# Kernel tuning notes

Hardware: AMD Instinct MI355X
Metric: run time of the kernel (lower is better)

The kernel has to match this reference:

```python
import jax, jax.numpy as jnp
import numpy as np

LEVELS = 2
BS = 8                 # block_size == plane_h == plane_w
NORMALS = (0, 1, 2)    # axis-aligned plane normals within each block
TAU = 0.05
INV_SQRT2 = 0.7071067811865476

# ---------- 1D orthonormal Haar along an axis ----------

def _dwt1(x, axis):
    x = jnp.moveaxis(x, axis, -1)
    a, b = x[..., 0::2], x[..., 1::2]
    lo = (a + b) * INV_SQRT2
    hi = (a - b) * INV_SQRT2
    return jnp.moveaxis(lo, -1, axis), jnp.moveaxis(hi, -1, axis)


def _idwt1(lo, hi, axis):
    lo = jnp.moveaxis(lo, axis, -1)
    hi = jnp.moveaxis(hi, axis, -1)
    even = (lo + hi) * INV_SQRT2
    odd = (lo - hi) * INV_SQRT2
    y = jnp.stack([even, odd], axis=-1).reshape(lo.shape[:-1] + (lo.shape[-1] * 2,))
    return jnp.moveaxis(y, -1, axis)

# ---------- one level of separable 3D Haar (8 subbands) ----------

def _dwt3_level(x):
    ld, hd = _dwt1(x, -3)
    out = {}
    for dn, db in (('l', ld), ('h', hd)):
        lh, hh = _dwt1(db, -2)
        for hn, hb in (('l', lh), ('h', hh)):
            lw, hw = _dwt1(hb, -1)
            out[dn + hn + 'l'] = lw
            out[dn + hn + 'h'] = hw
    return out


def _idwt3_level(bands):
    rec_h = {dn + hn: _idwt1(bands[dn + hn + 'l'], bands[dn + hn + 'h'], -1)
             for dn in 'lh' for hn in 'lh'}
    rec_d = {dn: _idwt1(rec_h[dn + 'l'], rec_h[dn + 'h'], -2) for dn in 'lh'}
    return _idwt1(rec_d['l'], rec_d['h'], -3)

# ---------- full multi-level 2D Haar on the last two dims (planes) ----------

def _haar2_fwd(p):
    s = p.shape[-1]
    out = p
    while s > 1:
        sub = out[..., :s, :s]
        a, b = sub[..., 0::2, :], sub[..., 1::2, :]
        sub = jnp.concatenate([(a + b) * INV_SQRT2, (a - b) * INV_SQRT2], axis=-2)
        a, b = sub[..., :, 0::2], sub[..., :, 1::2]
        sub = jnp.concatenate([(a + b) * INV_SQRT2, (a - b) * INV_SQRT2], axis=-1)
        out = out.at[..., :s, :s].set(sub)
        s //= 2
    return out


def _haar2_inv(c):
    s_full = c.shape[-1]
    out = c
    s = 2
    while s <= s_full:
        sub = out[..., :s, :s]
        lo, hi = sub[..., :, :s // 2], sub[..., :, s // 2:]
        even = (lo + hi) * INV_SQRT2
        odd = (lo - hi) * INV_SQRT2
        sub = jnp.stack([even, odd], axis=-1).reshape(sub.shape[:-1] + (s,))
        lo, hi = sub[..., :s // 2, :], sub[..., s // 2:, :]
        even = (lo + hi) * INV_SQRT2
        odd = (lo - hi) * INV_SQRT2
        sub = jnp.stack([even, odd], axis=-2).reshape(sub.shape[:-2] + (s, s))
        out = out.at[..., :s, :s].set(sub)
        s *= 2
    return out

# ---------- block extraction / assembly ----------

def _extract_blocks(band, bs):
    B, C, D, H, W = band.shape
    pd, ph, pw = (-D) % bs, (-H) % bs, (-W) % bs
    band = jnp.pad(band, ((0, 0), (0, 0), (0, pd), (0, ph), (0, pw)), mode='edge')
    nd, nh, nw = (D + pd) // bs, (H + ph) // bs, (W + pw) // bs
    blk = band.reshape(B, C, nd, bs, nh, bs, nw, bs).transpose(0, 1, 2, 4, 6, 3, 5, 7)
    return blk.reshape(-1, bs, bs, bs), (B, C, D, H, W), (nd, nh, nw)


def _assemble_blocks(blocks, orig, nblk, bs):
    B, C, D, H, W = orig
    nd, nh, nw = nblk
    x = blocks.reshape(B, C, nd, nh, nw, bs, bs, bs).transpose(0, 1, 2, 5, 3, 6, 4, 7)
    x = x.reshape(B, C, nd * bs, nh * bs, nw * bs)
    return x[:, :, :D, :H, :W]

# ---------- planewise bandlet analysis / synthesis ----------

def _analyze(blocks):
    # for each normal axis n: slice cube into planes perpendicular to n, 2D Haar each plane
    return jnp.stack([_haar2_fwd(jnp.moveaxis(blocks, 1 + n, 1)) for n in NORMALS], axis=1)


def _synthesize(packed):
    recs = [jnp.moveaxis(_haar2_inv(packed[:, i]), 1, 1 + n) for i, n in enumerate(NORMALS)]
    acc = recs[0]
    for r in recs[1:]:
        acc = acc + r
    return acc / len(NORMALS)


def _soft_threshold(c, tau):
    dc = c[..., 0, 0]  # keep per-plane DC coefficient
    t = jnp.sign(c) * jnp.maximum(jnp.abs(c) - tau, 0.0)
    return t.at[..., 0, 0].set(dc)

# ---------- full encode -> threshold -> reconstruct ----------

def _forward(x):
    B, C, D, H, W = x.shape
    mult = 2 ** LEVELS
    pd, ph, pw = (-D) % mult, (-H) % mult, (-W) % mult
    xp = jnp.pad(x, ((0, 0), (0, 0), (0, pd), (0, ph), (0, pw)), mode='reflect')
    approx = xp
    levels = []
    for _ in range(LEVELS):
        bands = _dwt3_level(approx)
        approx = bands.pop('lll')
        levels.append(bands)
    rec_levels = []
    for bands in levels:
        rec = {}
        for name, band in bands.items():
            blocks, orig, nblk = _extract_blocks(band, BS)
            packed = _soft_threshold(_analyze(blocks), TAU)
            rec[name] = _assemble_blocks(_synthesize(packed), orig, nblk, BS)
        rec_levels.append(rec)
    y = approx
    for bands in reversed(rec_levels):
        bands = dict(bands)
        bands['lll'] = y
        y = _idwt3_level(bands)
    return y[:, :, :D, :H, :W]


def setup_inputs() -> dict:
    key = jax.random.key(0)
    x = jax.random.normal(key, (2, 1, 160, 160, 160), dtype=jnp.float32)
    return {"x": x}


def reference(x):
    return _forward(x)
```

## Files before the change

### kernel.cpp

```cpp
#include <hip/hip_runtime.h>

#define IS2 0.7071067811865476f
#define C3F 0.35355339059327373f
#define TAU_F 0.05f
#define THIRD 0.3333333333333333f

__device__ __forceinline__ void haar2_fwd(float (&m)[64]) {
    #pragma unroll
    for (int half = 4; half >= 1; half >>= 1) {
        const int sz = half * 2;
        float th[32];
        #pragma unroll
        for (int r = 0; r < half; ++r)
            #pragma unroll
            for (int c = 0; c < sz; ++c) {
                float a = m[(2*r)*8 + c], b = m[(2*r+1)*8 + c];
                m[r*8 + c] = (a + b) * IS2;
                th[r*8 + c] = (a - b) * IS2;
            }
        #pragma unroll
        for (int r = 0; r < half; ++r)
            #pragma unroll
            for (int c = 0; c < sz; ++c) m[(r+half)*8 + c] = th[r*8 + c];
        #pragma unroll
        for (int r = 0; r < sz; ++r) {
            float tw[4];
            #pragma unroll
            for (int c = 0; c < half; ++c) {
                float a = m[r*8 + 2*c], b = m[r*8 + 2*c + 1];
                m[r*8 + c] = (a + b) * IS2;
                tw[c]      = (a - b) * IS2;
            }
            #pragma unroll
            for (int c = 0; c < half; ++c) m[r*8 + c + half] = tw[c];
        }
    }
}

__device__ __forceinline__ void haar2_inv(float (&m)[64]) {
    #pragma unroll
    for (int sz = 2; sz <= 8; sz <<= 1) {
        const int half = sz >> 1;
        #pragma unroll
        for (int r = 0; r < sz; ++r) {
            float te[8];
            #pragma unroll
            for (int c = 0; c < half; ++c) {
                float lo = m[r*8 + c], hi = m[r*8 + c + half];
                te[2*c]   = (lo + hi) * IS2;
                te[2*c+1] = (lo - hi) * IS2;
            }
            #pragma unroll
            for (int k = 0; k < sz; ++k) m[r*8 + k] = te[k];
        }
        #pragma unroll
        for (int c = 0; c < sz; ++c) {
            float tc[8];
            #pragma unroll
            for (int r = 0; r < half; ++r) {
                float lo = m[r*8 + c], hi = m[(r+half)*8 + c];
                tc[2*r]   = (lo + hi) * IS2;
                tc[2*r+1] = (lo - hi) * IS2;
            }
            #pragma unroll
            for (int r = 0; r < sz; ++r) m[r*8 + c] = tc[r];
        }
    }
}

__device__ __forceinline__ void bandlet_slice(float (&m)[64]) {
    haar2_fwd(m);
    float dc = m[0];
    #pragma unroll
    for (int e = 0; e < 64; ++e) {
        float v = m[e];
        float av = fabsf(v) - TAU_F;
        m[e] = av > 0.0f ? copysignf(av, v) : 0.0f;
    }
    m[0] = dc;
    haar2_inv(m);
}

__device__ __forceinline__ void blockproc3(float* __restrict__ Lb,
                                           float* __restrict__ Rb,
                                           int wv, int s, bool act,
                                           float (&m)[64]) {
    if (act) {
        if (wv == 0) {
            #pragma unroll
            for (int r = 0; r < 8; ++r) {
                float4 v0 = *(const float4*)&Lb[s*64 + r*8];
                float4 v1 = *(const float4*)&Lb[s*64 + r*8 + 4];
                m[r*8+0]=v0.x; m[r*8+1]=v0.y; m[r*8+2]=v0.z; m[r*8+3]=v0.w;
                m[r*8+4]=v1.x; m[r*8+5]=v1.y; m[r*8+6]=v1.z; m[r*8+7]=v1.w;
            }
        } else if (wv == 1) {
            #pragma unroll
            for (int r = 0; r < 8; ++r) {
                float4 v0 = *(const float4*)&Lb[r*64 + s*8];
                float4 v1 = *(const float4*)&Lb[r*64 + s*8 + 4];
                m[r*8+0]=v0.x; m[r*8+1]=v0.y; m[r*8+2]=v0.z; m[r*8+3]=v0.w;
                m[r*8+4]=v1.x; m[r*8+5]=v1.y; m[r*8+6]=v1.z; m[r*8+7]=v1.w;
            }
        } else {
            #pragma unroll
            for (int r = 0; r < 8; ++r)
                #pragma unroll
                for (int c = 0; c < 8; ++c)
                    m[r*8+c] = Lb[r*64 + c*8 + s];
        }
    }
    __syncthreads();
    if (act) {
        bandlet_slice(m);
        if (wv == 1) {
            #pragma unroll
            for (int r = 0; r < 8; ++r) {
                *(float4*)&Lb[r*64 + s*8]     = make_float4(m[r*8+0], m[r*8+1], m[r*8+2], m[r*8+3]);
                *(float4*)&Lb[r*64 + s*8 + 4] = make_float4(m[r*8+4], m[r*8+5], m[r*8+6], m[r*8+7]);
            }
        } else if (wv == 2) {
            #pragma unroll
            for (int r = 0; r < 8; ++r)
                #pragma unroll
                for (int c = 0; c < 8; ++c)
                    Rb[r*64 + c*8 + s] = m[r*8+c];
        }
    }
    __syncthreads();
    if (act && wv == 0) {
        #pragma unroll
        for (int r = 0; r < 8; ++r) {
            float4 a0 = *(const float4*)&Lb[s*64 + r*8];
            float4 a1 = *(const float4*)&Lb[s*64 + r*8 + 4];
            float4 b0 = *(const float4*)&Rb[s*64 + r*8];
            float4 b1 = *(const float4*)&Rb[s*64 + r*8 + 4];
            m[r*8+0] += a0.x + b0.x; m[r*8+1] += a0.y + b0.y;
            m[r*8+2] += a0.z + b0.z; m[r*8+3] += a0.w + b0.w;
            m[r*8+4] += a1.x + b1.x; m[r*8+5] += a1.y + b1.y;
            m[r*8+6] += a1.z + b1.z; m[r*8+7] += a1.w + b1.w;
        }
    }
}

__global__ __launch_bounds__(192, 4) void fwd1_bp(const float* __restrict__ x,
                                                  float* __restrict__ bands) {
    constexpr int LST = 516;
    constexpr size_t B1S = (size_t)2 * 80 * 80 * 80;
    __shared__ __align__(16) float lin[7 * LST];
    __shared__ __align__(16) float lr2[7 * LST];

    const int t  = threadIdx.x;
    const int wg = blockIdx.x;
    const int b  = wg / 1000;
    const int tl = wg - b * 1000;
    const int td = tl / 100;
    const int rr = tl - td * 100;
    const int th = rr / 10;
    const int tw = rr - th * 10;

    const float* ip = x + ((size_t)(b*160 + 16*td)) * 25600 + (size_t)(16*th) * 160 + 16*tw;
    float* lllp = bands + ((size_t)(b*80 + 8*td)) * 6400 + (size_t)(8*th) * 80 + 8*tw;

    #pragma unroll
    for (int k = 0; k < 3; ++k) {
        const int p = t + k * 192;
        if (p < 512) {
            const int q = p >> 6, j = (p >> 3) & 7, w = p & 7;
            const float* pp = ip + (size_t)(2*q) * 25600 + (2*j) * 160 + 2*w;
            float2 q00 = *(const float2*)(pp);
            float2 q01 = *(const float2*)(pp + 160);
            float2 q10 = *(const float2*)(pp + 25600);
            float2 q11 = *(const float2*)(pp + 25600 + 160);
            float wl00 = q00.x + q00.y, wh00 = q00.x - q00.y;
            float wl01 = q01.x + q01.y, wh01 = q01.x - q01.y;
            float wl10 = q10.x + q10.y, wh10 = q10.x - q10.y;
            float wl11 = q11.x + q11.y, wh11 = q11.x - q11.y;
            float hl0l = wl00 + wl01, hh0l = wl00 - wl01;
            float hl0h = wh00 + wh01, hh0h = wh00 - wh01;
            float hl1l = wl10 + wl11, hh1l = wl10 - wl11;
            float hl1h = wh10 + wh11, hh1h = wh10 - wh11;
            const int pos = q*64 + j*8 + w;
            lin[0*LST + pos] = (hl0h + hl1h) * C3F;
            lin[1*LST + pos] = (hh0l + hh1l) * C3F;
            lin[2*LST + pos] = (hh0h + hh1h) * C3F;
            lin[3*LST + pos] = (hl0l - hl1l) * C3F;
            lin[4*LST + pos] = (hl0h - hl1h) * C3F;
            lin[5*LST + pos] = (hh0l - hh1l) * C3F;
            lin[6*LST + pos] = (hh0h - hh1h) * C3F;
            lllp[q*6400 + j*80 + w] = (hl0l + hl1l) * C3F;
        }
    }
    __syncthreads();

    const int wv   = t >> 6;
    const int lane = t & 63;
    const int f    = lane >> 3;
    const int s    = lane & 7;
    const bool act = f < 7;
    const int fc   = act ? f : 0;

    float m[64];
    blockproc3(&lin[fc * LST], &lr2[fc * LST], wv, s, act, m);

    if (act && wv == 0) {
        float* gp = bands + (size_t)(f + 1) * B1S
                  + ((size_t)(b*80 + 8*td + s)) * 6400 + (size_t)(8*th) * 80 + 8*tw;
        #pragma unroll
        for (int jj = 0; jj < 8; ++jj) {
            float* qo = gp + jj * 80;
            *(float4*)(qo)     = make_float4(m[jj*8+0]*THIRD, m[jj*8+1]*THIRD,
                                             m[jj*8+2]*THIRD, m[jj*8+3]*THIRD);
            *(float4*)(qo + 4) = make_float4(m[jj*8+4]*THIRD, m[jj*8+5]*THIRD,
                                             m[jj*8+6]*THIRD, m[jj*8+7]*THIRD);
        }
    }
}

__global__ __launch_bounds__(192, 4) void l2_pipeline(float* __restrict__ lll) {
    constexpr int LST = 516;
    __shared__ __align__(16) float lin[8 * LST];
    __shared__ __align__(16) float lr2[7 * LST];

    const int t  = threadIdx.x;
    const int wg = blockIdx.x;
    const int b  = wg / 125;
    const int tl = wg - b * 125;
    const int td = tl / 25;
    const int rr = tl - td * 25;
    const int th = rr / 5;
    const int tw = rr - th * 5;

    float* base = lll + ((size_t)(b*80 + 16*td)) * 6400 + (size_t)(16*th) * 80 + 16*tw;

    #pragma unroll
    for (int k = 0; k < 3; ++k) {
        const int p = t + k * 192;
        if (p < 512) {
            const int q = p >> 6, j = (p >> 3) & 7, w = p & 7;
            const float* pp = base + (size_t)(2*q) * 6400 + (2*j) * 80 + 2*w;
            float2 q00 = *(const float2*)(pp);
            float2 q01 = *(const float2*)(pp + 80);
            float2 q10 = *(const float2*)(pp + 6400);
            float2 q11 = *(const float2*)(pp + 6400 + 80);
            float wl00 = q00.x + q00.y, wh00 = q00.x - q00.y;
            float wl01 = q01.x + q01.y, wh01 = q01.x - q01.y;
            float wl10 = q10.x + q10.y, wh10 = q10.x - q10.y;
            float wl11 = q11.x + q11.y, wh11 = q11.x - q11.y;
            float hl0l = wl00 + wl01, hh0l = wl00 - wl01;
            float hl0h = wh00 + wh01, hh0h = wh00 - wh01;
            float hl1l = wl10 + wl11, hh1l = wl10 - wl11;
            float hl1h = wh10 + wh11, hh1h = wh10 - wh11;
            const int pos = q*64 + j*8 + w;
            lin[0*LST + pos] = (hl0l + hl1l) * C3F;
            lin[1*LST + pos] = (hl0h + hl1h) * C3F;
            lin[2*LST + pos] = (hh0l + hh1l) * C3F;
            lin[3*LST + pos] = (hh0h + hh1h) * C3F;
            lin[4*LST + pos] = (hl0l - hl1l) * C3F;
            lin[5*LST + pos] = (hl0h - hl1h) * C3F;
            lin[6*LST + pos] = (hh0l - hh1l) * C3F;
            lin[7*LST + pos] = (hh0h - hh1h) * C3F;
        }
    }
    __syncthreads();

    const int wv   = t >> 6;
    const int lane = t & 63;
    const int f    = lane >> 3;
    const int s    = lane & 7;
    const bool act = f < 7;

    float m[64];
    blockproc3(&lin[(act ? f + 1 : 1) * LST], &lr2[(act ? f : 0) * LST], wv, s, act, m);

    if (act && wv == 0) {
        float* Lb = &lin[(f + 1) * LST];
        #pragma unroll
        for (int r = 0; r < 8; ++r) {
            *(float4*)&Lb[s*64 + r*8]     = make_float4(m[r*8+0]*THIRD, m[r*8+1]*THIRD,
                                                        m[r*8+2]*THIRD, m[r*8+3]*THIRD);
            *(float4*)&Lb[s*64 + r*8 + 4] = make_float4(m[r*8+4]*THIRD, m[r*8+5]*THIRD,
                                                        m[r*8+6]*THIRD, m[r*8+7]*THIRD);
        }
    }
    __syncthreads();

    #pragma unroll
    for (int k = 0; k < 3; ++k) {
        const int p = t + k * 192;
        if (p < 512) {
            const int q = p >> 6, j = (p >> 3) & 7, w = p & 7;
            const int pos = q*64 + j*8 + w;
            float b0 = lin[0*LST + pos], b1 = lin[1*LST + pos];
            float b2 = lin[2*LST + pos], b3 = lin[3*LST + pos];
            float b4 = lin[4*LST + pos], b5 = lin[5*LST + pos];
            float b6 = lin[6*LST + pos], b7 = lin[7*LST + pos];
            float c0 = b0 + b4, c1 = b1 + b5, c2 = b2 + b6, c3 = b3 + b7;
            float c4 = b0 - b4, c5 = b1 - b5, c6 = b2 - b6, c7 = b3 - b7;
            float e00 = c0 + c2, e01 = c1 + c3;
            float e02 = c0 - c2, e03 = c1 - c3;
            float e10 = c4 + c6, e11 = c5 + c7;
            float e12 = c4 - c6, e13 = c5 - c7;
            float* pp = base + (size_t)(2*q) * 6400 + (2*j) * 80 + 2*w;
            *(float2*)(pp)             = make_float2((e00+e01)*C3F, (e00-e01)*C3F);
            *(float2*)(pp + 80)        = make_float2((e02+e03)*C3F, (e02-e03)*C3F);
            *(float2*)(pp + 6400)      = make_float2((e10+e11)*C3F, (e10-e11)*C3F);
            *(float2*)(pp + 6400 + 80) = make_float2((e12+e13)*C3F, (e12-e13)*C3F);
        }
    }
}

__global__ __launch_bounds__(256) void dwt3_inv80(const float* __restrict__ bands,
                                                  float* __restrict__ out) {
    const int tid = blockIdx.x * blockDim.x + threadIdx.x;
    constexpr int S = 80;
    constexpr size_t bs_ = (size_t)2 * S * S * S;
    const size_t o = (size_t)tid * 2;
    const int w = (int)(o % S);
    const int h = (int)((o / S) % S);
    const int d = (int)((o / (S*S)) % S);
    const int b = (int)(o / ((size_t)S*S*S));

    float2 B0 = *(const float2*)&bands[0*bs_ + o];
    float2 B1 = *(const float2*)&bands[1*bs_ + o];
    float2 B2 = *(const float2*)&bands[2*bs_ + o];
    float2 B3 = *(const float2*)&bands[3*bs_ + o];
    float2 B4 = *(const float2*)&bands[4*bs_ + o];
    float2 B5 = *(const float2*)&bands[5*bs_ + o];
    float2 B6 = *(const float2*)&bands[6*bs_ + o];
    float2 B7 = *(const float2*)&bands[7*bs_ + o];

    float c0x = B0.x + B4.x, c1x = B1.x + B5.x, c2x = B2.x + B6.x, c3x = B3.x + B7.x;
    float c4x = B0.x - B4.x, c5x = B1.x - B5.x, c6x = B2.x - B6.x, c7x = B3.x - B7.x;
    float e00x = c0x + c2x, e01x = c1x + c3x, e02x = c0x - c2x, e03x = c1x - c3x;
    float e10x = c4x + c6x, e11x = c5x + c7x, e12x = c4x - c6x, e13x = c5x - c7x;

    float c0y = B0.y + B4.y, c1y = B1.y + B5.y, c2y = B2.y + B6.y, c3y = B3.y + B7.y;
    float c4y = B0.y - B4.y, c5y = B1.y - B5.y, c6y = B2.y - B6.y, c7y = B3.y - B7.y;
    float e00y = c0y + c2y, e01y = c1y + c3y, e02y = c0y - c2y, e03y = c1y - c3y;
    float e10y = c4y + c6y, e11y = c5y + c7y, e12y = c4y - c6y, e13y = c5y - c7y;

    float* p = out + (((size_t)b * 160 + 2*d) * 160 + 2*h) * 160 + 2*w;
    *(float4*)(p)               = make_float4((e00x+e01x)*C3F, (e00x-e01x)*C3F,
                                              (e00y+e01y)*C3F, (e00y-e01y)*C3F);
    *(float4*)(p + 160)         = make_float4((e02x+e03x)*C3F, (e02x-e03x)*C3F,
                                              (e02y+e03y)*C3F, (e02y-e03y)*C3F);
    *(float4*)(p + 25600)       = make_float4((e10x+e11x)*C3F, (e10x-e11x)*C3F,
                                              (e10y+e11y)*C3F, (e10y-e11y)*C3F);
    *(float4*)(p + 25600 + 160) = make_float4((e12x+e13x)*C3F, (e12x-e13x)*C3F,
                                              (e12y+e13y)*C3F, (e12y-e13y)*C3F);
}

extern "C" void kernel_launch(void* const* d_in, const int* in_sizes, int n_in,
                              void* d_out, int out_size, void* d_ws, size_t ws_size,
                              hipStream_t stream) {
    const float* x = (const float*)d_in[0];
    float* out = (float*)d_out;
    float* bands = (float*)d_ws;

    fwd1_bp<<<2000, 192, 0, stream>>>(x, bands);
    l2_pipeline<<<250, 192, 0, stream>>>(bands);
    dwt3_inv80<<<2000, 256, 0, stream>>>(bands, out);
}
```

Baseline: 120.3 us.

## Store level-1 bands in blocked 8x8x8 layout and switch inverse to nontemporal stores

The intermediate band workspace is changed from a plain 80^3 volume layout to a block-contiguous layout where each 8x8x8 block occupies 512 consecutive floats. Level-1 writes become fully contiguous, the level-2 pipeline gathers and scatters with block-index arithmetic, and the final inverse kernel processes two blocks per workgroup, writing output with nontemporal stores. The goal is more contiguous memory transactions and less cache pollution from the output write. In exchange the level-2 accesses become more scattered and the index math more complex.

```diff
diff --git a/kernel.cpp b/kernel.cpp
--- a/kernel.cpp
+++ b/kernel.cpp
@@ -4,6 +4,8 @@
 #define C3F 0.35355339059327373f
 #define TAU_F 0.05f
 #define THIRD 0.3333333333333333f
+
+typedef float floatx4 __attribute__((ext_vector_type(4)));
 
 __device__ __forceinline__ void haar2_fwd(float (&m)[64]) {
     #pragma unroll
@@ -143,10 +145,10 @@
     }
 }
 
+
 __global__ __launch_bounds__(192, 4) void fwd1_bp(const float* __restrict__ x,
                                                   float* __restrict__ bands) {
     constexpr int LST = 516;
-    constexpr size_t B1S = (size_t)2 * 80 * 80 * 80;
     __shared__ __align__(16) float lin[7 * LST];
     __shared__ __align__(16) float lr2[7 * LST];
 
@@ -160,7 +162,7 @@
     const int tw = rr - th * 10;
 
     const float* ip = x + ((size_t)(b*160 + 16*td)) * 25600 + (size_t)(16*th) * 160 + 16*tw;
-    float* lllp = bands + ((size_t)(b*80 + 8*td)) * 6400 + (size_t)(8*th) * 80 + 8*tw;
+    float* lllp = bands + ((size_t)(0*2 + b) * 1000 + tl) * 512;
 
     #pragma unroll
     for (int k = 0; k < 3; ++k) {
@@ -180,15 +182,14 @@
             float hl0h = wh00 + wh01, hh0h = wh00 - wh01;
             float hl1l = wl10 + wl11, hh1l = wl10 - wl11;
             float hl1h = wh10 + wh11, hh1h = wh10 - wh11;
-            const int pos = q*64 + j*8 + w;
-            lin[0*LST + pos] = (hl0h + hl1h) * C3F;
-            lin[1*LST + pos] = (hh0l + hh1l) * C3F;
-            lin[2*LST + pos] = (hh0h + hh1h) * C3F;
-            lin[3*LST + pos] = (hl0l - hl1l) * C3F;
-            lin[4*LST + pos] = (hl0h - hl1h) * C3F;
-            lin[5*LST + pos] = (hh0l - hh1l) * C3F;
-            lin[6*LST + pos] = (hh0h - hh1h) * C3F;
-            lllp[q*6400 + j*80 + w] = (hl0l + hl1l) * C3F;
+            lin[0*LST + p] = (hl0h + hl1h) * C3F;
+            lin[1*LST + p] = (hh0l + hh1l) * C3F;
+            lin[2*LST + p] = (hh0h + hh1h) * C3F;
+            lin[3*LST + p] = (hl0l - hl1l) * C3F;
+            lin[4*LST + p] = (hl0h - hl1h) * C3F;
+            lin[5*LST + p] = (hh0l - hh1l) * C3F;
+            lin[6*LST + p] = (hh0h - hh1h) * C3F;
+            lllp[p] = (hl0l + hl1l) * C3F;
         }
     }
     __syncthreads();
@@ -204,20 +205,16 @@
     blockproc3(&lin[fc * LST], &lr2[fc * LST], wv, s, act, m);
 
     if (act && wv == 0) {
-        float* gp = bands + (size_t)(f + 1) * B1S
-                  + ((size_t)(b*80 + 8*td + s)) * 6400 + (size_t)(8*th) * 80 + 8*tw;
-        #pragma unroll
-        for (int jj = 0; jj < 8; ++jj) {
-            float* qo = gp + jj * 80;
-            *(float4*)(qo)     = make_float4(m[jj*8+0]*THIRD, m[jj*8+1]*THIRD,
-                                             m[jj*8+2]*THIRD, m[jj*8+3]*THIRD);
-            *(float4*)(qo + 4) = make_float4(m[jj*8+4]*THIRD, m[jj*8+5]*THIRD,
-                                             m[jj*8+6]*THIRD, m[jj*8+7]*THIRD);
-        }
-    }
-}
-
-__global__ __launch_bounds__(192, 4) void l2_pipeline(float* __restrict__ lll) {
+        float* base = bands + ((size_t)((f + 1)*2 + b) * 1000 + tl) * 512 + s * 64;
+        #pragma unroll
+        for (int e = 0; e < 16; ++e) {
+            *(float4*)&base[e*4] = make_float4(m[e*4+0]*THIRD, m[e*4+1]*THIRD,
+                                               m[e*4+2]*THIRD, m[e*4+3]*THIRD);
+        }
+    }
+}
+
+__global__ __launch_bounds__(192, 4) void l2_pipeline(float* __restrict__ bands) {
     constexpr int LST = 516;
     __shared__ __align__(16) float lin[8 * LST];
     __shared__ __align__(16) float lr2[7 * LST];
@@ -231,35 +228,42 @@
     const int th = rr / 5;
     const int tw = rr - th * 5;
 
-    float* base = lll + ((size_t)(b*80 + 16*td)) * 6400 + (size_t)(16*th) * 80 + 16*tw;
+    float* band0 = bands + (size_t)b * 1000 * 512;
 
     #pragma unroll
     for (int k = 0; k < 3; ++k) {
         const int p = t + k * 192;
         if (p < 512) {
             const int q = p >> 6, j = (p >> 3) & 7, w = p & 7;
-            const float* pp = base + (size_t)(2*q) * 6400 + (2*j) * 80 + 2*w;
-            float2 q00 = *(const float2*)(pp);
-            float2 q01 = *(const float2*)(pp + 80);
-            float2 q10 = *(const float2*)(pp + 6400);
-            float2 q11 = *(const float2*)(pp + 6400 + 80);
-            float wl00 = q00.x + q00.y, wh00 = q00.x - q00.y;
-            float wl01 = q01.x + q01.y, wh01 = q01.x - q01.y;
-            float wl10 = q10.x + q10.y, wh10 = q10.x - q10.y;
-            float wl11 = q11.x + q11.y, wh11 = q11.x - q11.y;
+            const int e_ = w >> 2;
+            const int kk = (2*w) & 7;
+            float2 v[2][2];
+            #pragma unroll
+            for (int dz = 0; dz < 2; ++dz) {
+                const int d = 2*q + dz, a = d >> 3, i = d & 7;
+                #pragma unroll
+                for (int dy = 0; dy < 2; ++dy) {
+                    const int h = 2*j + dy, c = h >> 3, jj = h & 7;
+                    const size_t blk = (size_t)(2*td + a) * 100 + (2*th + c) * 10 + (2*tw + e_);
+                    v[dz][dy] = *(const float2*)&band0[blk * 512 + i*64 + jj*8 + kk];
+                }
+            }
+            float wl00 = v[0][0].x + v[0][0].y, wh00 = v[0][0].x - v[0][0].y;
+            float wl01 = v[0][1].x + v[0][1].y, wh01 = v[0][1].x - v[0][1].y;
+            float wl10 = v[1][0].x + v[1][0].y, wh10 = v[1][0].x - v[1][0].y;
+            float wl11 = v[1][1].x + v[1][1].y, wh11 = v[1][1].x - v[1][1].y;
             float hl0l = wl00 + wl01, hh0l = wl00 - wl01;
             float hl0h = wh00 + wh01, hh0h = wh00 - wh01;
             float hl1l = wl10 + wl11, hh1l = wl10 - wl11;
             float hl1h = wh10 + wh11, hh1h = wh10 - wh11;
-            const int pos = q*64 + j*8 + w;
-            lin[0*LST + pos] = (hl0l + hl1l) * C3F;
-            lin[1*LST + pos] = (hl0h + hl1h) * C3F;
-            lin[2*LST + pos] = (hh0l + hh1l) * C3F;
-            lin[3*LST + pos] = (hh0h + hh1h) * C3F;
-            lin[4*LST + pos] = (hl0l - hl1l) * C3F;
-            lin[5*LST + pos] = (hl0h - hl1h) * C3F;
-            lin[6*LST + pos] = (hh0l - hh1l) * C3F;
-            lin[7*LST + pos] = (hh0h - hh1h) * C3F;
+            lin[0*LST + p] = (hl0l + hl1l) * C3F;
+            lin[1*LST + p] = (hl0h + hl1h) * C3F;
+            lin[2*LST + p] = (hh0l + hh1l) * C3F;
+            lin[3*LST + p] = (hh0h + hh1h) * C3F;
+            lin[4*LST + p] = (hl0l - hl1l) * C3F;
+            lin[5*LST + p] = (hl0h - hl1h) * C3F;
+            lin[6*LST + p] = (hh0l - hh1l) * C3F;
+            lin[7*LST + p] = (hh0h - hh1h) * C3F;
         }
     }
     __syncthreads();
@@ -290,65 +294,90 @@
         const int p = t + k * 192;
         if (p < 512) {
             const int q = p >> 6, j = (p >> 3) & 7, w = p & 7;
-            const int pos = q*64 + j*8 + w;
-            float b0 = lin[0*LST + pos], b1 = lin[1*LST + pos];
-            float b2 = lin[2*LST + pos], b3 = lin[3*LST + pos];
-            float b4 = lin[4*LST + pos], b5 = lin[5*LST + pos];
-            float b6 = lin[6*LST + pos], b7 = lin[7*LST + pos];
+            float b0 = lin[0*LST + p], b1 = lin[1*LST + p];
+            float b2 = lin[2*LST + p], b3 = lin[3*LST + p];
+            float b4 = lin[4*LST + p], b5 = lin[5*LST + p];
+            float b6 = lin[6*LST + p], b7 = lin[7*LST + p];
             float c0 = b0 + b4, c1 = b1 + b5, c2 = b2 + b6, c3 = b3 + b7;
             float c4 = b0 - b4, c5 = b1 - b5, c6 = b2 - b6, c7 = b3 - b7;
             float e00 = c0 + c2, e01 = c1 + c3;
             float e02 = c0 - c2, e03 = c1 - c3;
             float e10 = c4 + c6, e11 = c5 + c7;
             float e12 = c4 - c6, e13 = c5 - c7;
-            float* pp = base + (size_t)(2*q) * 6400 + (2*j) * 80 + 2*w;
-            *(float2*)(pp)             = make_float2((e00+e01)*C3F, (e00-e01)*C3F);
-            *(float2*)(pp + 80)        = make_float2((e02+e03)*C3F, (e02-e03)*C3F);
-            *(float2*)(pp + 6400)      = make_float2((e10+e11)*C3F, (e10-e11)*C3F);
-            *(float2*)(pp + 6400 + 80) = make_float2((e12+e13)*C3F, (e12-e13)*C3F);
+            const int e_ = w >> 2;
+            const int kk = (2*w) & 7;
+            #pragma unroll
+            for (int dz = 0; dz < 2; ++dz) {
+                const int d = 2*q + dz, a = d >> 3, i = d & 7;
+                const float ex0 = dz ? e10 : e00, ex1 = dz ? e11 : e01;
+                const float ex2 = dz ? e12 : e02, ex3 = dz ? e13 : e03;
+                #pragma unroll
+                for (int dy = 0; dy < 2; ++dy) {
+                    const int h = 2*j + dy, c = h >> 3, jj = h & 7;
+                    const float lo = dy ? ex2 : ex0, hi = dy ? ex3 : ex1;
+                    const size_t blk = (size_t)(2*td + a) * 100 + (2*th + c) * 10 + (2*tw + e_);
+                    *(float2*)&band0[blk * 512 + i*64 + jj*8 + kk] =
+                        make_float2((lo + hi) * C3F, (lo - hi) * C3F);
+                }
+            }
         }
     }
 }
 
 __global__ __launch_bounds__(256) void dwt3_inv80(const float* __restrict__ bands,
                                                   float* __restrict__ out) {
-    const int tid = blockIdx.x * blockDim.x + threadIdx.x;
-    constexpr int S = 80;
-    constexpr size_t bs_ = (size_t)2 * S * S * S;
-    const size_t o = (size_t)tid * 2;
-    const int w = (int)(o % S);
-    const int h = (int)((o / S) % S);
-    const int d = (int)((o / (S*S)) % S);
-    const int b = (int)(o / ((size_t)S*S*S));
-
-    float2 B0 = *(const float2*)&bands[0*bs_ + o];
-    float2 B1 = *(const float2*)&bands[1*bs_ + o];
-    float2 B2 = *(const float2*)&bands[2*bs_ + o];
-    float2 B3 = *(const float2*)&bands[3*bs_ + o];
-    float2 B4 = *(const float2*)&bands[4*bs_ + o];
-    float2 B5 = *(const float2*)&bands[5*bs_ + o];
-    float2 B6 = *(const float2*)&bands[6*bs_ + o];
-    float2 B7 = *(const float2*)&bands[7*bs_ + o];
-
-    float c0x = B0.x + B4.x, c1x = B1.x + B5.x, c2x = B2.x + B6.x, c3x = B3.x + B7.x;
-    float c4x = B0.x - B4.x, c5x = B1.x - B5.x, c6x = B2.x - B6.x, c7x = B3.x - B7.x;
-    float e00x = c0x + c2x, e01x = c1x + c3x, e02x = c0x - c2x, e03x = c1x - c3x;
-    float e10x = c4x + c6x, e11x = c5x + c7x, e12x = c4x - c6x, e13x = c5x - c7x;
-
-    float c0y = B0.y + B4.y, c1y = B1.y + B5.y, c2y = B2.y + B6.y, c3y = B3.y + B7.y;
-    float c4y = B0.y - B4.y, c5y = B1.y - B5.y, c6y = B2.y - B6.y, c7y = B3.y - B7.y;
-    float e00y = c0y + c2y, e01y = c1y + c3y, e02y = c0y - c2y, e03y = c1y - c3y;
-    float e10y = c4y + c6y, e11y = c5y + c7y, e12y = c4y - c6y, e13y = c5y - c7y;
-
-    float* p = out + (((size_t)b * 160 + 2*d) * 160 + 2*h) * 160 + 2*w;
-    *(float4*)(p)               = make_float4((e00x+e01x)*C3F, (e00x-e01x)*C3F,
-                                              (e00y+e01y)*C3F, (e00y-e01y)*C3F);
-    *(float4*)(p + 160)         = make_float4((e02x+e03x)*C3F, (e02x-e03x)*C3F,
-                                              (e02y+e03y)*C3F, (e02y-e03y)*C3F);
-    *(float4*)(p + 25600)       = make_float4((e10x+e11x)*C3F, (e10x-e11x)*C3F,
-                                              (e10y+e11y)*C3F, (e10y-e11y)*C3F);
-    *(float4*)(p + 25600 + 160) = make_float4((e12x+e13x)*C3F, (e12x-e13x)*C3F,
-                                              (e12y+e13y)*C3F, (e12y-e13y)*C3F);
+    const int t  = threadIdx.x;
+    const int wg = blockIdx.x;
+    const int b   = wg / 500;
+    const int r0  = wg - b * 500;
+    const int Bd  = r0 / 50;
+    const int r1  = r0 - Bd * 50;
+    const int Bh  = r1 / 5;
+    const int Bwp = r1 - Bh * 5;
+
+    const int p0 = 2 * t;
+    const int q  = p0 >> 6, j = (p0 >> 3) & 7, w0 = p0 & 7;
+
+    #pragma unroll
+    for (int e = 0; e < 2; ++e) {
+        const int Bw = 2 * Bwp + e;
+        const size_t blk = (size_t)Bd * 100 + Bh * 10 + Bw;
+
+        float2 B0, B1, B2, B3, B4, B5, B6, B7;
+        {
+            const float* bp = bands + ((size_t)b * 1000 + blk) * 512 + p0;
+            constexpr size_t FS = (size_t)2 * 1000 * 512;
+            B0 = *(const float2*)(bp + 0*FS);
+            B1 = *(const float2*)(bp + 1*FS);
+            B2 = *(const float2*)(bp + 2*FS);
+            B3 = *(const float2*)(bp + 3*FS);
+            B4 = *(const float2*)(bp + 4*FS);
+            B5 = *(const float2*)(bp + 5*FS);
+            B6 = *(const float2*)(bp + 6*FS);
+            B7 = *(const float2*)(bp + 7*FS);
+        }
+
+        float c0x = B0.x + B4.x, c1x = B1.x + B5.x, c2x = B2.x + B6.x, c3x = B3.x + B7.x;
+        float c4x = B0.x - B4.x, c5x = B1.x - B5.x, c6x = B2.x - B6.x, c7x = B3.x - B7.x;
+        float e00x = c0x + c2x, e01x = c1x + c3x, e02x = c0x - c2x, e03x = c1x - c3x;
+        float e10x = c4x + c6x, e11x = c5x + c7x, e12x = c4x - c6x, e13x = c5x - c7x;
+
+        float c0y = B0.y + B4.y, c1y = B1.y + B5.y, c2y = B2.y + B6.y, c3y = B3.y + B7.y;
+        float c4y = B0.y - B4.y, c5y = B1.y - B5.y, c6y = B2.y - B6.y, c7y = B3.y - B7.y;
+        float e00y = c0y + c2y, e01y = c1y + c3y, e02y = c0y - c2y, e03y = c1y - c3y;
+        float e10y = c4y + c6y, e11y = c5y + c7y, e12y = c4y - c6y, e13y = c5y - c7y;
+
+        float* p = out + (((size_t)b * 160 + 16*Bd + 2*q) * 160 + 16*Bh + 2*j) * 160
+                       + 16*Bw + 2*w0;
+        floatx4 o0 = { (e00x+e01x)*C3F, (e00x-e01x)*C3F, (e00y+e01y)*C3F, (e00y-e01y)*C3F };
+        floatx4 o1 = { (e02x+e03x)*C3F, (e02x-e03x)*C3F, (e02y+e03y)*C3F, (e02y-e03y)*C3F };
+        floatx4 o2 = { (e10x+e11x)*C3F, (e10x-e11x)*C3F, (e10y+e11y)*C3F, (e10y-e11y)*C3F };
+        floatx4 o3 = { (e12x+e13x)*C3F, (e12x-e13x)*C3F, (e12y+e13y)*C3F, (e12y-e13y)*C3F };
+        __builtin_nontemporal_store(o0, (floatx4*)(p));
+        __builtin_nontemporal_store(o1, (floatx4*)(p + 160));
+        __builtin_nontemporal_store(o2, (floatx4*)(p + 25600));
+        __builtin_nontemporal_store(o3, (floatx4*)(p + 25600 + 160));
+    }
 }
 
 extern "C" void kernel_launch(void* const* d_in, const int* in_sizes, int n_in,
@@ -360,5 +389,5 @@
 
     fwd1_bp<<<2000, 192, 0, stream>>>(x, bands);
     l2_pipeline<<<250, 192, 0, stream>>>(bands);
-    dwt3_inv80<<<2000, 256, 0, stream>>>(bands, out);
-}
+    dwt3_inv80<<<1000, 256, 0, stream>>>(bands, out);
+}
```

After: 117.6 us. 1.02x faster.
